# Kernel tuning notes

Hardware: AMD Instinct MI355X
Metric: run time of the kernel (lower is better)

The kernel has to match this reference:

```python
import jax, jax.numpy as jnp
import numpy as np

B, S, E, H, DK = 4, 1024, 1024, 16, 64
FF = 2048
SCALE = int(np.sqrt(DK))  # source uses int(np.sqrt(keySize)) = 8
EPS = 1e-5


def _mha(x_kv, x_q, Wq, Wk, Wv, Wo, mask):
    # Wq/Wk/Wv: [H, E, DK]; Wo: [H*DK, E]
    k = jnp.einsum('bse,hed->hbsd', x_kv, Wk)   # [H,B,S,DK]
    v = jnp.einsum('bse,hed->hbsd', x_kv, Wv)
    q = jnp.einsum('bse,hed->hbsd', x_q, Wq)
    # source does keys.reshape(B, DK, S) -- a RAW reshape, not a transpose
    kR = k.reshape(H, B, DK, S)
    scores = jnp.einsum('hbsd,hbdt->hbst', q, kR)  # [H,B,S,S]
    if mask is not None:
        scores = scores + mask  # mask added BEFORE the scale divide, as in source
    att = jax.nn.softmax(scores / SCALE, axis=-1)
    out = jnp.einsum('hbst,hbtd->hbsd', att, v)    # [H,B,S,DK]
    # source stacks heads then does a RAW reshape [H,B,S,DK] -> [B,S,DK*H]
    out = out.reshape(B, S, DK * H)
    return out @ Wo  # [B,S,E]


def _layernorm2d(x, w, b):
    # LayerNorm over last two dims (S, E) with affine params [S, E]
    m = jnp.mean(x, axis=(-2, -1), keepdims=True)
    v = jnp.var(x, axis=(-2, -1), keepdims=True)
    return (x - m) * jax.lax.rsqrt(v + EPS) * w + b


def setup_inputs() -> dict:
    key = jax.random.key(0)
    ks = jax.random.split(key, 24)
    u = lambda k, shp: jax.random.uniform(k, shp, dtype=jnp.float32)  # weights ~ U(0,1) as in source
    inp = {
        'inputRes': jax.random.normal(ks[0], (B, S, E), dtype=jnp.float32),
        'outputEncoding': jax.random.normal(ks[1], (B, S, E), dtype=jnp.float32),
        'Wq1': u(ks[2], (H, E, DK)), 'Wk1': u(ks[3], (H, E, DK)), 'Wv1': u(ks[4], (H, E, DK)),
        'Wo1': u(ks[5], (H * DK, E)),
        'Wq2': u(ks[6], (H, E, DK)), 'Wk2': u(ks[7], (H, E, DK)), 'Wv2': u(ks[8], (H, E, DK)),
        'Wo2': u(ks[9], (H * DK, E)),
        'ln1_w': jnp.ones((S, E), jnp.float32), 'ln1_b': jnp.zeros((S, E), jnp.float32),
        'ln2_w': jnp.ones((S, E), jnp.float32), 'ln2_b': jnp.zeros((S, E), jnp.float32),
        'ln3_w': jnp.ones((S, E), jnp.float32), 'ln3_b': jnp.zeros((S, E), jnp.float32),
        'W1': jax.random.normal(ks[10], (S, FF), dtype=jnp.float32) * (1.0 / np.sqrt(S)),
        'b1': jnp.zeros((FF,), jnp.float32),
        'W2': jax.random.normal(ks[11], (FF, S), dtype=jnp.float32) * (1.0 / np.sqrt(FF)),
        'b2': jnp.zeros((S,), jnp.float32),
    }
    return inp


def reference(inputRes, outputEncoding, Wq1, Wk1, Wv1, Wo1, Wq2, Wk2, Wv2, Wo2,
              ln1_w, ln1_b, ln2_w, ln2_b, ln3_w, ln3_b, W1, b1, W2, b2):
    # causal mask: row i has 0 for j<=i, -inf for j>i
    idx = jnp.arange(S)
    mask = jnp.where(idx[None, :] <= idx[:, None], 0.0, -jnp.inf).astype(jnp.float32)

    # masked self-attention + residual + LN1
    att = _mha(outputEncoding, outputEncoding, Wq1, Wk1, Wv1, Wo1, mask)
    att_norm = _layernorm2d(att + outputEncoding, ln1_w, ln1_b)

    # cross-attention (K,V from inputRes; Q from att_norm) + residual to outputEncoding + LN2
    att2 = _mha(inputRes, att_norm, Wq2, Wk2, Wv2, Wo2, None)
    att2_norm = _layernorm2d(att2 + outputEncoding, ln2_w, ln2_b)

    # FFN over the sequence dim via RAW reshape (B,S,E)->(B,E,S), as in source
    norm_res = att2_norm.reshape(B, E, S)
    fc = jax.nn.relu(norm_res @ W1 + b1) @ W2 + b2  # [B,E,S]
    fc = fc.reshape(B, S, E)

    return _layernorm2d(fc + att2_norm, ln3_w, ln3_b)
```

## Files before the change

kernel.cpp:

```cpp
#include <hip/hip_runtime.h>
#include <cstdint>
#include <cstddef>


#define DI __device__ __forceinline__
#define MFMA __builtin_amdgcn_mfma_f32_16x16x32_bf16

typedef short s8v __attribute__((ext_vector_type(8)));
typedef float f4v __attribute__((ext_vector_type(4)));
typedef unsigned u4v __attribute__((ext_vector_type(4)));

DI float bf2f(short u){
  union { unsigned int i; float f; } v;
  v.i = ((unsigned int)(unsigned short)u) << 16;
  return v.f;
}
DI short f2bf(float f){
  union { float f; unsigned int i; } v; v.f = f;
  unsigned int x = v.i;
  return (short)((x + 0x7fffu + ((x >> 16) & 1u)) >> 16);
}
DI unsigned pack2(short hi, short lo){
  return ((unsigned)(unsigned short)lo << 16) | (unsigned)(unsigned short)hi;
}
DI unsigned packf(float val){
  short hi = f2bf(val);
  return pack2(hi, f2bf(val - bf2f(hi)));
}
DI void gload16(const void* g, void* l){
  __builtin_amdgcn_global_load_lds(
      (const __attribute__((address_space(1))) unsigned*)g,
      (__attribute__((address_space(3))) unsigned*)l, 16, 0, 0);
}

struct SplitP { const float* src[2]; short* hi[2]; short* lo[2]; };

__launch_bounds__(256)
__global__ void splitall_k(SplitP sp){
  const int t = blockIdx.y;
  int i = (blockIdx.x * 256 + threadIdx.x) << 2;
  float4 v = *(const float4*)(sp.src[t] + i);
  float xs[4] = {v.x, v.y, v.z, v.w};
  short h[4], l[4];
  #pragma unroll
  for (int c = 0; c < 4; c++){
    h[c] = f2bf(xs[c]);
    l[c] = f2bf(xs[c] - bf2f(h[c]));
  }
  *(short4*)(sp.hi[t] + i) = make_short4(h[0], h[1], h[2], h[3]);
  *(short4*)(sp.lo[t] + i) = make_short4(l[0], l[1], l[2], l[3]);
}

struct TransP {
  const float* src[10];
  short* oh[10]; short* ol[10];
  int Kd[10]; int Nd[10]; int qkv[10]; int ntiles[10];
};

__launch_bounds__(256)
__global__ void transall_k(TransP tp){
  const int t = blockIdx.y;
  const int tile = blockIdx.x;
  if (tile >= tp.ntiles[t]) return;
  const int K = tp.Kd[t], N = tp.Nd[t];
  const int ncols = N >> 6;
  const int n0 = (tile % ncols) << 6, k0 = (tile / ncols) << 6;
  __shared__ float Ld[64 * 65];
  const int tid = threadIdx.x;
  const int row = tid >> 2, c16 = (tid & 3) << 4;
  const float* s = tp.src[t];
  size_t base;
  if (tp.qkv[t]) base = ((size_t)(n0 >> 6) << 16) + ((size_t)(k0 + row) << 6) + c16;
  else           base = (size_t)(k0 + row) * N + n0 + c16;
  #pragma unroll
  for (int j4 = 0; j4 < 4; j4++){
    float4 v = *(const float4*)(s + base + (j4 << 2));
    int c = row * 65 + c16 + (j4 << 2);
    Ld[c] = v.x; Ld[c + 1] = v.y; Ld[c + 2] = v.z; Ld[c + 3] = v.w;
  }
  __syncthreads();
  const int n = tid >> 2;
  s8v h0, h1, l0, l1;
  #pragma unroll
  for (int j = 0; j < 8; j++){
    float a = Ld[(c16 + j) * 65 + n];
    float b = Ld[(c16 + 8 + j) * 65 + n];
    short ha = f2bf(a), hb = f2bf(b);
    h0[j] = ha; l0[j] = f2bf(a - bf2f(ha));
    h1[j] = hb; l1[j] = f2bf(b - bf2f(hb));
  }
  size_t ob = (size_t)(n0 + n) * K + k0 + c16;
  *(s8v*)(tp.oh[t] + ob)     = h0;
  *(s8v*)(tp.oh[t] + ob + 8) = h1;
  *(s8v*)(tp.ol[t] + ob)     = l0;
  *(s8v*)(tp.ol[t] + ob + 8) = l1;
}

struct GemmP {
  const short* Ah; const short* Al; int lda;
  const short* Bh; const short* Bl; int ldb;
  int K; int N;
  const float* xres; const float* bias;
  float* outf;
  short* o1h; short* o1l;
  unsigned* p1; unsigned* p2; unsigned* p3;
};

template<int TM, int EPI, int TERMS>
__launch_bounds__(512, 2)
__global__ void gemm_k(GemmP p){
  constexpr int AGR = TM * 4;
  constexpr int NGRAN = (TERMS == 3 ? 2 * AGR : AGR) + 1024;
  constexpr int NG = NGRAN >> 9;
  constexpr int WM = TM >> 6;
  constexpr int NB = 128 / (8 / WM) / 16;
  __shared__ short AhL[3][TM * 32];
  __shared__ short AlL[3][(TERMS == 3) ? TM * 32 : 8];
  __shared__ short BhL[3][128 * 32];
  __shared__ short BlL[3][128 * 32];
  const int tid = threadIdx.x;
  const int L = tid & 63, w = tid >> 6;
  const int lr = L & 15, lg = L >> 4;
  const int mo = (w & (WM - 1)) << 6;
  const int no = (w / WM) * (NB << 4);

  const int gx = gridDim.x, gy = gridDim.y;
  const int f = blockIdx.y * gx + blockIdx.x;
  const int j = f >> 3;
  const int jm = j / gx;
  const int mb = (f & 7) * (gy >> 3) + jm;
  const int nb = j - jm * gx;
  const int m0 = mb * TM, n0 = nb << 7;

  const int lrow4 = L >> 2, lq = L & 3;

  int aoff[4], boff[NB];
  #pragma unroll
  for (int mi = 0; mi < 4; mi++){
    int r = mo + (mi << 4) + lr;
    aoff[mi] = (r << 5) + ((lg ^ ((r >> 1) & 3)) << 3);
  }
  #pragma unroll
  for (int ni = 0; ni < NB; ni++){
    int n = no + (ni << 4) + lr;
    boff[ni] = (n << 5) + ((lg ^ ((n >> 1) & 3)) << 3);
  }

  f4v acc[4][NB];
  #pragma unroll
  for (int i = 0; i < 4; i++)
    #pragma unroll
    for (int jj = 0; jj < NB; jj++)
      #pragma unroll
      for (int r = 0; r < 4; r++) acc[i][jj][r] = 0.0f;

  const int nkt = p.K >> 5;

  auto stage = [&](int tile, int slot){
    const int k0 = tile << 5;
    #pragma unroll
    for (int i = 0; i < NG; i++){
      int base_c = (i << 9) + (w << 6);
      const short* plane; short* lds; int row0; int ld; int pc;
      if (base_c < AGR){
        pc = base_c; plane = p.Ah; lds = &AhL[slot][0]; row0 = m0; ld = p.lda;
      } else if (TERMS == 3 && base_c < 2 * AGR){
        pc = base_c - AGR; plane = p.Al; lds = &AlL[slot][0]; row0 = m0; ld = p.lda;
      } else {
        int pc2 = base_c - (TERMS == 3 ? 2 * AGR : AGR);
        if (pc2 < 512){ pc = pc2; plane = p.Bh; lds = &BhL[slot][0]; }
        else          { pc = pc2 - 512; plane = p.Bl; lds = &BlL[slot][0]; }
        row0 = n0; ld = p.ldb;
      }
      int rl = (pc >> 2) + lrow4;
      int sc = (lq ^ ((rl >> 1) & 3)) << 3;
      gload16(plane + (size_t)(row0 + rl) * ld + k0 + sc, lds + (pc << 3));
    }
  };

  stage(0, 0);
  stage(1, 1);

  for (int kt = 0; kt < nkt; kt++){
    const int cur = kt % 3;
    asm volatile("s_waitcnt vmcnt(%0)\n\ts_barrier" :: "i"(NG) : "memory");

    s8v a_h[4], a_l[4], b_h[NB], b_l[NB];
    #pragma unroll
    for (int mi = 0; mi < 4; mi++){
      a_h[mi] = *(const s8v*)&AhL[cur][aoff[mi]];
      if (TERMS == 3) a_l[mi] = *(const s8v*)&AlL[cur][aoff[mi]];
    }
    #pragma unroll
    for (int ni = 0; ni < NB; ni++){
      b_h[ni] = *(const s8v*)&BhL[cur][boff[ni]];
      b_l[ni] = *(const s8v*)&BlL[cur][boff[ni]];
    }

    int nt = kt + 2 < nkt ? kt + 2 : nkt - 1;
    stage(nt, (kt + 2) % 3);

    #pragma unroll
    for (int ni = 0; ni < NB; ni++){
      #pragma unroll
      for (int mi = 0; mi < 4; mi++){
        acc[mi][ni] = MFMA(a_h[mi], b_h[ni], acc[mi][ni], 0, 0, 0);
        acc[mi][ni] = MFMA(a_h[mi], b_l[ni], acc[mi][ni], 0, 0, 0);
        if (TERMS == 3)
          acc[mi][ni] = MFMA(a_l[mi], b_h[ni], acc[mi][ni], 0, 0, 0);
      }
    }
  }

  #pragma unroll
  for (int mi = 0; mi < 4; mi++){
    #pragma unroll
    for (int ni = 0; ni < NB; ni++){
      #pragma unroll
      for (int r = 0; r < 4; r++){
        float val = acc[mi][ni][r];
        int m = m0 + mo + (mi << 4) + (lg << 2) + r;
        int n = n0 + no + (ni << 4) + lr;
        if (EPI == 2){
          size_t o = (size_t)m * p.N + n;
          p.outf[o] = val + p.xres[o];
        } else if (EPI == 4){
          p.outf[(size_t)m * p.N + n] = val + p.bias[n];
        } else if (EPI == 3){
          float x = val + p.bias[n];
          x = x > 0.0f ? x : 0.0f;
          size_t o = (size_t)m * p.N + n;
          short hi = f2bf(x);
          p.o1h[o] = hi;
          p.o1l[o] = f2bf(x - bf2f(hi));
        } else {
          int seg = (EPI == 0) ? 0 : (n >> 10);
          int n1 = (EPI == 0) ? n : (n & 1023);
          int kind = (EPI == 0) ? 0 : (EPI == 6 ? seg : seg + 1);
          int b = m >> 10, s = m & 1023, hh = n1 >> 6, d = n1 & 63;
          size_t hb16 = (size_t)((hh << 2) | b) << 16;
          size_t dst;
          if (kind == 0)      dst = hb16 + ((size_t)s << 6) + d;
          else if (kind == 1) dst = hb16 + ((size_t)(((s & 15) << 6) | d) << 6) + (s >> 4);
          else                dst = hb16 + ((size_t)d << 10) + s;
          unsigned* dp = (EPI == 0) ? p.p1
                       : (EPI == 6) ? (seg == 0 ? p.p1 : (seg == 1 ? p.p2 : p.p3))
                                    : (seg == 0 ? p.p1 : p.p2);
          dp[dst] = packf(val);
        }
      }
    }
  }
}

template<int CAUSAL>
__launch_bounds__(256, 2)
__global__ void flash_k(const unsigned* __restrict__ qpk,
                        const unsigned* __restrict__ kpk,
                        const unsigned* __restrict__ vpk,
                        short* __restrict__ ohi_g, short* __restrict__ olo_g){
  __shared__ short Kt[2][64*72];
  __shared__ short Vt[2][64*72];
  __shared__ unsigned Ps[2][4][16*68];
  const int tid = threadIdx.x, L = tid & 63, w = tid >> 6;
  const int lr = L & 15, lg = L >> 4;
  const int flat = blockIdx.x + (blockIdx.y << 3);
  const int hb = ((flat & 7) << 3) | ((flat >> 3) & 7);
  const int sp = flat >> 6;
  const int h = hb >> 2, b = hb & 3;
  const size_t hbo = (size_t)hb << 16;
  const float NEG_INF = -__builtin_inff();
  int qt[2]; qt[0] = sp; qt[1] = CAUSAL ? (15 - sp) : (sp + 8);

  s8v qfh[2][2], qfl[2][2];
  #pragma unroll
  for (int st = 0; st < 2; st++){
    const unsigned* qg = qpk + hbo + (size_t)((qt[st] << 6) + (w << 4) + lr) * 64 + (lg << 3);
    #pragma unroll
    for (int ks = 0; ks < 2; ks++){
      u4v p0 = *(const u4v*)(qg + (ks << 5));
      u4v p1 = *(const u4v*)(qg + (ks << 5) + 4);
      #pragma unroll
      for (int jj = 0; jj < 4; jj++){
        qfh[st][ks][jj]     = (short)(p0[jj] & 0xffffu);
        qfl[st][ks][jj]     = (short)(p0[jj] >> 16);
        qfh[st][ks][4 + jj] = (short)(p1[jj] & 0xffffu);
        qfl[st][ks][4 + jj] = (short)(p1[jj] >> 16);
      }
    }
  }

  f4v o[2][4];
  float mprev[2][4], lsum[2][4];
  #pragma unroll
  for (int st = 0; st < 2; st++){
    #pragma unroll
    for (int ni = 0; ni < 4; ni++)
      #pragma unroll
      for (int r = 0; r < 4; r++) o[st][ni][r] = 0.0f;
    #pragma unroll
    for (int r = 0; r < 4; r++){ mprev[st][r] = NEG_INF; lsum[st][r] = 0.0f; }
  }

  const int ntt = CAUSAL ? (qt[1] + 1) : 16;
  for (int ti = 0; ti < ntt; ti++){
    const int t0 = ti << 6;
    const bool actA = !(CAUSAL && ti > qt[0]);
    __syncthreads();
    {
      const int row = tid >> 2, col = (tid & 3) << 4;
      const unsigned* kg = kpk + hbo + (size_t)(t0 + row) * 64 + col;
      const unsigned* vg = vpk + hbo + ((size_t)row << 10) + t0 + col;
      unsigned kb[16], vb[16];
      #pragma unroll
      for (int j4 = 0; j4 < 4; j4++){
        *(u4v*)&kb[j4 << 2] = *(const u4v*)(kg + (j4 << 2));
        *(u4v*)&vb[j4 << 2] = *(const u4v*)(vg + (j4 << 2));
      }
      s8v kh0, kh1, kl0, kl1, vh0, vh1, vl0, vl1;
      #pragma unroll
      for (int jj = 0; jj < 8; jj++){
        kh0[jj] = (short)(kb[jj] & 0xffffu);      kl0[jj] = (short)(kb[jj] >> 16);
        kh1[jj] = (short)(kb[8 + jj] & 0xffffu);  kl1[jj] = (short)(kb[8 + jj] >> 16);
        vh0[jj] = (short)(vb[jj] & 0xffffu);      vl0[jj] = (short)(vb[jj] >> 16);
        vh1[jj] = (short)(vb[8 + jj] & 0xffffu);  vl1[jj] = (short)(vb[8 + jj] >> 16);
      }
      const int lb = row * 72 + col;
      *(s8v*)&Kt[0][lb] = kh0;  *(s8v*)&Kt[0][lb + 8] = kh1;
      *(s8v*)&Kt[1][lb] = kl0;  *(s8v*)&Kt[1][lb + 8] = kl1;
      *(s8v*)&Vt[0][lb] = vh0;  *(s8v*)&Vt[0][lb + 8] = vh1;
      *(s8v*)&Vt[1][lb] = vl0;  *(s8v*)&Vt[1][lb + 8] = vl1;
    }
    __syncthreads();

    f4v sa[2][4];
    #pragma unroll
    for (int st = 0; st < 2; st++)
      #pragma unroll
      for (int ni = 0; ni < 4; ni++)
        #pragma unroll
        for (int r = 0; r < 4; r++) sa[st][ni][r] = 0.0f;
    #pragma unroll
    for (int ks = 0; ks < 2; ks++){
      const int kb = (ks << 5) + (lg << 3);
      #pragma unroll
      for (int ni = 0; ni < 4; ni++){
        const int tl = (ni << 4) + lr;
        s8v kbh = *(const s8v*)&Kt[0][tl * 72 + kb];
        s8v kbl = *(const s8v*)&Kt[1][tl * 72 + kb];
        if (actA){
          sa[0][ni] = MFMA(qfh[0][ks], kbh, sa[0][ni], 0, 0, 0);
          sa[0][ni] = MFMA(qfh[0][ks], kbl, sa[0][ni], 0, 0, 0);
          sa[0][ni] = MFMA(qfl[0][ks], kbh, sa[0][ni], 0, 0, 0);
        }
        sa[1][ni] = MFMA(qfh[1][ks], kbh, sa[1][ni], 0, 0, 0);
        sa[1][ni] = MFMA(qfh[1][ks], kbl, sa[1][ni], 0, 0, 0);
        sa[1][ni] = MFMA(qfl[1][ks], kbh, sa[1][ni], 0, 0, 0);
      }
    }

    #pragma unroll
    for (int st = 0; st < 2; st++){
      if (st == 0 && !actA) continue;
      const int s0w = (qt[st] << 6) + (w << 4);
      const bool diag = CAUSAL && (ti == qt[st]);
      float tm[4] = {NEG_INF, NEG_INF, NEG_INF, NEG_INF};
      #pragma unroll
      for (int ni = 0; ni < 4; ni++)
        #pragma unroll
        for (int r = 0; r < 4; r++){
          float v = sa[st][ni][r] * 0.125f;
          if (diag){
            int tg = t0 + (ni << 4) + lr;
            int sg = s0w + (lg << 2) + r;
            if (tg > sg) v = NEG_INF;
          }
          sa[st][ni][r] = v;
          tm[r] = fmaxf(tm[r], v);
        }
      #pragma unroll
      for (int off = 1; off < 16; off <<= 1)
        #pragma unroll
        for (int r = 0; r < 4; r++) tm[r] = fmaxf(tm[r], __shfl_xor(tm[r], off, 16));
      float alpha[4], psum[4];
      #pragma unroll
      for (int r = 0; r < 4; r++){
        float mn = fmaxf(mprev[st][r], tm[r]);
        alpha[r] = __expf(mprev[st][r] - mn);
        mprev[st][r] = mn;
        psum[r] = 0.0f;
      }
      #pragma unroll
      for (int ni = 0; ni < 4; ni++)
        #pragma unroll
        for (int r = 0; r < 4; r++){
          float pv = __expf(sa[st][ni][r] - mprev[st][r]);
          sa[st][ni][r] = pv;
          psum[r] += pv;
        }
      #pragma unroll
      for (int off = 1; off < 16; off <<= 1)
        #pragma unroll
        for (int r = 0; r < 4; r++) psum[r] += __shfl_xor(psum[r], off, 16);
      #pragma unroll
      for (int r = 0; r < 4; r++) lsum[st][r] = lsum[st][r] * alpha[r] + psum[r];
      #pragma unroll
      for (int ni = 0; ni < 4; ni++)
        #pragma unroll
        for (int r = 0; r < 4; r++) o[st][ni][r] *= alpha[r];
      #pragma unroll
      for (int ni = 0; ni < 4; ni++)
        #pragma unroll
        for (int r = 0; r < 4; r++){
          int prow = (lg << 2) + r, pcol = (ni << 4) + lr;
          Ps[st][w][prow * 68 + pcol] = packf(sa[st][ni][r]);
        }
    }

    #pragma unroll
    for (int ks = 0; ks < 2; ks++){
      const int kb = (ks << 5) + (lg << 3);
      s8v ph[2], pl[2];
      #pragma unroll
      for (int st = 0; st < 2; st++){
        if (st == 0 && !actA) continue;
        u4v p0 = *(const u4v*)&Ps[st][w][lr * 68 + kb];
        u4v p1 = *(const u4v*)&Ps[st][w][lr * 68 + kb + 4];
        #pragma unroll
        for (int jj = 0; jj < 4; jj++){
          ph[st][jj]     = (short)(p0[jj] & 0xffffu);  pl[st][jj]     = (short)(p0[jj] >> 16);
          ph[st][4 + jj] = (short)(p1[jj] & 0xffffu);  pl[st][4 + jj] = (short)(p1[jj] >> 16);
        }
      }
      #pragma unroll
      for (int ni = 0; ni < 4; ni++){
        const int d = (ni << 4) + lr;
        s8v vbh = *(const s8v*)&Vt[0][d * 72 + kb];
        s8v vbl = *(const s8v*)&Vt[1][d * 72 + kb];
        if (actA){
          o[0][ni] = MFMA(ph[0], vbh, o[0][ni], 0, 0, 0);
          o[0][ni] = MFMA(ph[0], vbl, o[0][ni], 0, 0, 0);
          o[0][ni] = MFMA(pl[0], vbh, o[0][ni], 0, 0, 0);
        }
        o[1][ni] = MFMA(ph[1], vbh, o[1][ni], 0, 0, 0);
        o[1][ni] = MFMA(ph[1], vbl, o[1][ni], 0, 0, 0);
        o[1][ni] = MFMA(pl[1], vbh, o[1][ni], 0, 0, 0);
      }
    }
  }

  #pragma unroll
  for (int st = 0; st < 2; st++){
    const int s0w = (qt[st] << 6) + (w << 4);
    #pragma unroll
    for (int ni = 0; ni < 4; ni++){
      #pragma unroll
      for (int r = 0; r < 4; r++){
        float val = o[st][ni][r] / lsum[st][r];
        int s = s0w + (lg << 2) + r;
        int d = (ni << 4) + lr;
        int s2i = ((h & 3) << 8) | (b << 6) | (s >> 4);
        int c   = ((s & 15) << 6) | d;
        size_t dst = ((size_t)(h >> 2) << 20) + ((size_t)s2i << 10) + c;
        short hi = f2bf(val);
        ohi_g[dst] = hi;
        olo_g[dst] = f2bf(val - bf2f(hi));
      }
    }
  }
}

__launch_bounds__(256)
__global__ void ln_partial_k(const float* s1, const float* s2, float2* part){
  const int tid = threadIdx.x, L = tid & 63, w = tid >> 6;
  const int b = blockIdx.y, j = blockIdx.x;
  const size_t base = ((size_t)b << 20) + ((size_t)j << 13) + ((size_t)tid << 2);
  float sum = 0.0f, ss = 0.0f;
  #pragma unroll
  for (int i = 0; i < 8; i++){
    size_t idx = base + ((size_t)i << 10);
    float4 v = *(const float4*)(s1 + idx);
    if (s2){
      float4 u = *(const float4*)(s2 + idx);
      v.x += u.x; v.y += u.y; v.z += u.z; v.w += u.w;
    }
    sum += v.x + v.y + v.z + v.w;
    ss  += v.x*v.x + v.y*v.y + v.z*v.z + v.w*v.w;
  }
  #pragma unroll
  for (int off = 1; off < 64; off <<= 1){
    sum += __shfl_xor(sum, off, 64);
    ss  += __shfl_xor(ss,  off, 64);
  }
  __shared__ float red[4][2];
  if (L == 0){ red[w][0] = sum; red[w][1] = ss; }
  __syncthreads();
  if (tid == 0){
    float s_ = red[0][0] + red[1][0] + red[2][0] + red[3][0];
    float q_ = red[0][1] + red[1][1] + red[2][1] + red[3][1];
    part[b * 128 + j] = make_float2(s_, q_);
  }
}

__launch_bounds__(64)
__global__ void ln_final_k(const float2* part, float2* stats){
  const int b = blockIdx.x, t = threadIdx.x;
  float2 a = part[b * 128 + t], c = part[b * 128 + 64 + t];
  float sum = a.x + c.x, ss = a.y + c.y;
  #pragma unroll
  for (int off = 1; off < 64; off <<= 1){
    sum += __shfl_xor(sum, off, 64);
    ss  += __shfl_xor(ss,  off, 64);
  }
  if (t == 0){
    float mean = sum * (1.0f / 1048576.0f);
    float var  = ss  * (1.0f / 1048576.0f) - mean * mean;
    stats[b] = make_float2(mean, rsqrtf(var + 1e-5f));
  }
}

template<int MODE>
__launch_bounds__(256)
__global__ void ln_apply_k(const float* s1, const float* s2,
                           const float* wgt, const float* bias,
                           const float2* stats,
                           float* dstf, short* dsta, short* dstb){
  const int tid = threadIdx.x;
  const size_t base = ((size_t)blockIdx.x << 11) + ((size_t)tid << 2);
  #pragma unroll
  for (int i = 0; i < 2; i++){
    size_t idx = base + ((size_t)i << 10);
    int b = (int)(idx >> 20);
    float2 st = stats[b];
    float4 x = *(const float4*)(s1 + idx);
    if (s2){
      float4 u = *(const float4*)(s2 + idx);
      x.x += u.x; x.y += u.y; x.z += u.z; x.w += u.w;
    }
    unsigned wi = (unsigned)(idx & 1048575u);
    float4 wv = *(const float4*)(wgt + wi);
    float4 bv = *(const float4*)(bias + wi);
    float xv[4] = {x.x, x.y, x.z, x.w};
    float wvv[4] = {wv.x, wv.y, wv.z, wv.w};
    float bvv[4] = {bv.x, bv.y, bv.z, bv.w};
    float yv[4];
    #pragma unroll
    for (int c = 0; c < 4; c++)
      yv[c] = (xv[c] - st.x) * st.y * wvv[c] + bvv[c];
    if (MODE == 0 || MODE == 1){
      short h[4], l[4];
      #pragma unroll
      for (int c = 0; c < 4; c++){
        h[c] = f2bf(yv[c]);
        l[c] = f2bf(yv[c] - bf2f(h[c]));
      }
      *(short4*)(dsta + idx) = make_short4(h[0], h[1], h[2], h[3]);
      *(short4*)(dstb + idx) = make_short4(l[0], l[1], l[2], l[3]);
      if (MODE == 1)
        *(float4*)(dstf + idx) = make_float4(yv[0], yv[1], yv[2], yv[3]);
    } else {
      *(float4*)(dstf + idx) = make_float4(yv[0], yv[1], yv[2], yv[3]);
    }
  }
}

extern "C" void kernel_launch(void* const* d_in, const int* in_sizes, int n_in,
                              void* d_out, int out_size, void* d_ws, size_t ws_size,
                              hipStream_t stream){
  const float* IRf = (const float*)d_in[0];
  const float* OEf = (const float*)d_in[1];
  const float* Wq1f = (const float*)d_in[2];
  const float* Wk1f = (const float*)d_in[3];
  const float* Wv1f = (const float*)d_in[4];
  const float* Wo1f = (const float*)d_in[5];
  const float* Wq2f = (const float*)d_in[6];
  const float* Wk2f = (const float*)d_in[7];
  const float* Wv2f = (const float*)d_in[8];
  const float* Wo2f = (const float*)d_in[9];
  const float* ln1w = (const float*)d_in[10];
  const float* ln1b = (const float*)d_in[11];
  const float* ln2w = (const float*)d_in[12];
  const float* ln2b = (const float*)d_in[13];
  const float* ln3w = (const float*)d_in[14];
  const float* ln3b = (const float*)d_in[15];
  const float* W1f = (const float*)d_in[16];
  const float* b1f = (const float*)d_in[17];
  const float* W2f = (const float*)d_in[18];
  const float* b2f = (const float*)d_in[19];
  float* dout = (float*)d_out;

  char* ws = (char*)d_ws;
  const size_t MB = (size_t)1 << 20;
  short* OEh = (short*)(ws + 0*MB),  *OEl = (short*)(ws + 8*MB);
  short* IRh = (short*)(ws + 16*MB), *IRl = (short*)(ws + 24*MB);
  short* QKV1t_h = (short*)(ws + 32*MB), *QKV1t_l = (short*)(ws + 38*MB);
  short* Wo1t_h  = (short*)(ws + 44*MB), *Wo1t_l  = (short*)(ws + 46*MB);
  short* Q2t_h   = (short*)(ws + 48*MB), *Q2t_l   = (short*)(ws + 50*MB);
  short* KV2t_h  = (short*)(ws + 52*MB), *KV2t_l  = (short*)(ws + 56*MB);
  short* Wo2t_h  = (short*)(ws + 60*MB), *Wo2t_l  = (short*)(ws + 62*MB);
  short* W1t_h   = (short*)(ws + 64*MB), *W1t_l   = (short*)(ws + 68*MB);
  short* W2t_h   = (short*)(ws + 72*MB), *W2t_l   = (short*)(ws + 76*MB);
  unsigned* q_pk = (unsigned*)(ws + 80*MB);
  unsigned* k_pk = (unsigned*)(ws + 96*MB);
  unsigned* v_pk = (unsigned*)(ws + 112*MB);
  short* outr_h = (short*)(ws + 128*MB), *outr_l = (short*)(ws + 136*MB);
  float* resid = (float*)(ws + 144*MB);
  short* attn_h = (short*)(ws + 160*MB), *attn_l = (short*)(ws + 168*MB);
  float* att2n_f = (float*)(ws + 176*MB);
  short* hid_h = (short*)(ws + 80*MB);
  short* hid_l = (short*)(ws + 96*MB);
  float* fc    = (float*)(ws + 112*MB);
  short* a2n_h = (short*)(ws + 160*MB);
  short* a2n_l = (short*)(ws + 168*MB);
  float2* part  = (float2*)(ws + 192*MB);
  float2* stats = (float2*)(ws + 192*MB + 65536);

  dim3 blk(256), blkg(512);

  SplitP sp;
  sp.src[0] = OEf; sp.hi[0] = OEh; sp.lo[0] = OEl;
  sp.src[1] = IRf; sp.hi[1] = IRh; sp.lo[1] = IRl;
  splitall_k<<<dim3(4096, 2), blk, 0, stream>>>(sp);

  TransP tp;
  const float* tsrc[10] = {Wq1f, Wk1f, Wv1f, Wo1f, Wq2f, Wk2f, Wv2f, Wo2f, W1f, W2f};
  short* toh[10] = {QKV1t_h, QKV1t_h + (1<<20), QKV1t_h + (2<<20), Wo1t_h,
                    Q2t_h, KV2t_h, KV2t_h + (1<<20), Wo2t_h, W1t_h, W2t_h};
  short* tol[10] = {QKV1t_l, QKV1t_l + (1<<20), QKV1t_l + (2<<20), Wo1t_l,
                    Q2t_l, KV2t_l, KV2t_l + (1<<20), Wo2t_l, W1t_l, W2t_l};
  int tK[10]   = {1024,1024,1024,1024,1024,1024,1024,1024,1024,2048};
  int tN[10]   = {1024,1024,1024,1024,1024,1024,1024,1024,2048,1024};
  int tq[10]   = {1,1,1,0,1,1,1,0,0,0};
  int tt[10]   = {256,256,256,256,256,256,256,256,512,512};
  for (int i = 0; i < 10; i++){
    tp.src[i] = tsrc[i]; tp.oh[i] = toh[i]; tp.ol[i] = tol[i];
    tp.Kd[i] = tK[i]; tp.Nd[i] = tN[i]; tp.qkv[i] = tq[i]; tp.ntiles[i] = tt[i];
  }
  transall_k<<<dim3(512, 10), blk, 0, stream>>>(tp);

  GemmP p{};

  p = {OEh, OEl, 1024, QKV1t_h, QKV1t_l, 1024, 1024, 3072, nullptr, nullptr,
       nullptr, nullptr, nullptr, q_pk, k_pk, v_pk};
  gemm_k<256,6,3><<<dim3(24, 16), blkg, 0, stream>>>(p);
  flash_k<1><<<dim3(8, 64), blk, 0, stream>>>(q_pk, k_pk, v_pk, outr_h, outr_l);
  p = {outr_h, outr_l, 1024, Wo1t_h, Wo1t_l, 1024, 1024, 1024, OEf, nullptr,
       resid, nullptr, nullptr, nullptr, nullptr, nullptr};
  gemm_k<128,2,3><<<dim3(8, 32), blkg, 0, stream>>>(p);
  ln_partial_k<<<dim3(128, 4), blk, 0, stream>>>(resid, nullptr, part);
  ln_final_k<<<dim3(4), dim3(64), 0, stream>>>(part, stats);
  ln_apply_k<0><<<dim3(2048), blk, 0, stream>>>(resid, nullptr, ln1w, ln1b, stats, nullptr, attn_h, attn_l);

  p = {attn_h, attn_l, 1024, Q2t_h, Q2t_l, 1024, 1024, 1024, nullptr, nullptr,
       nullptr, nullptr, nullptr, q_pk, nullptr, nullptr};
  gemm_k<128,0,3><<<dim3(8, 32), blkg, 0, stream>>>(p);
  p = {IRh, IRl, 1024, KV2t_h, KV2t_l, 1024, 1024, 2048, nullptr, nullptr,
       nullptr, nullptr, nullptr, k_pk, v_pk, nullptr};
  gemm_k<256,7,3><<<dim3(16, 16), blkg, 0, stream>>>(p);
  flash_k<0><<<dim3(8, 64), blk, 0, stream>>>(q_pk, k_pk, v_pk, outr_h, outr_l);
  p = {outr_h, outr_l, 1024, Wo2t_h, Wo2t_l, 1024, 1024, 1024, OEf, nullptr,
       resid, nullptr, nullptr, nullptr, nullptr, nullptr};
  gemm_k<128,2,3><<<dim3(8, 32), blkg, 0, stream>>>(p);
  ln_partial_k<<<dim3(128, 4), blk, 0, stream>>>(resid, nullptr, part);
  ln_final_k<<<dim3(4), dim3(64), 0, stream>>>(part, stats);
  ln_apply_k<1><<<dim3(2048), blk, 0, stream>>>(resid, nullptr, ln2w, ln2b, stats, att2n_f, a2n_h, a2n_l);

  p = {a2n_h, a2n_l, 1024, W1t_h, W1t_l, 1024, 1024, 2048, nullptr, b1f,
       nullptr, hid_h, hid_l, nullptr, nullptr, nullptr};
  gemm_k<256,3,2><<<dim3(16, 16), blkg, 0, stream>>>(p);
  p = {hid_h, hid_l, 2048, W2t_h, W2t_l, 2048, 2048, 1024, nullptr, b2f,
       fc, nullptr, nullptr, nullptr, nullptr, nullptr};
  gemm_k<128,4,2><<<dim3(8, 32), blkg, 0, stream>>>(p);
  ln_partial_k<<<dim3(128, 4), blk, 0, stream>>>(fc, att2n_f, part);
  ln_final_k<<<dim3(4), dim3(64), 0, stream>>>(part, stats);
  ln_apply_k<2><<<dim3(2048), blk, 0, stream>>>(fc, att2n_f, ln3w, ln3b, stats, dout, nullptr, nullptr);
}
```

Baseline: 690.7 us.

## Add 128x128 256-thread GEMM variant with double buffering for wide GEMMs

Adds a new GEMM kernel using 128x128 tiles, 256 threads (4 waves, each computing 64x64) and two-stage LDS buffering with a full vmcnt(0) wait. The QKV1, KV2 and FFN1 projections switch from the 256-row, 512-thread triple-buffered kernel to it, doubling the grid. The goal is more blocks per CU and better wave balance across CUs with less LDS per block. In exchange, the pipeline is shallower and the kernel waits for all loads every iteration, which may expose memory latency. The epilogue is moved into a shared helper.

```diff
diff --git a/kernel.cpp b/kernel.cpp
--- a/kernel.cpp
+++ b/kernel.cpp
@@ -106,112 +106,9 @@
   unsigned* p1; unsigned* p2; unsigned* p3;
 };
 
-template<int TM, int EPI, int TERMS>
-__launch_bounds__(512, 2)
-__global__ void gemm_k(GemmP p){
-  constexpr int AGR = TM * 4;
-  constexpr int NGRAN = (TERMS == 3 ? 2 * AGR : AGR) + 1024;
-  constexpr int NG = NGRAN >> 9;
-  constexpr int WM = TM >> 6;
-  constexpr int NB = 128 / (8 / WM) / 16;
-  __shared__ short AhL[3][TM * 32];
-  __shared__ short AlL[3][(TERMS == 3) ? TM * 32 : 8];
-  __shared__ short BhL[3][128 * 32];
-  __shared__ short BlL[3][128 * 32];
-  const int tid = threadIdx.x;
-  const int L = tid & 63, w = tid >> 6;
-  const int lr = L & 15, lg = L >> 4;
-  const int mo = (w & (WM - 1)) << 6;
-  const int no = (w / WM) * (NB << 4);
-
-  const int gx = gridDim.x, gy = gridDim.y;
-  const int f = blockIdx.y * gx + blockIdx.x;
-  const int j = f >> 3;
-  const int jm = j / gx;
-  const int mb = (f & 7) * (gy >> 3) + jm;
-  const int nb = j - jm * gx;
-  const int m0 = mb * TM, n0 = nb << 7;
-
-  const int lrow4 = L >> 2, lq = L & 3;
-
-  int aoff[4], boff[NB];
-  #pragma unroll
-  for (int mi = 0; mi < 4; mi++){
-    int r = mo + (mi << 4) + lr;
-    aoff[mi] = (r << 5) + ((lg ^ ((r >> 1) & 3)) << 3);
-  }
-  #pragma unroll
-  for (int ni = 0; ni < NB; ni++){
-    int n = no + (ni << 4) + lr;
-    boff[ni] = (n << 5) + ((lg ^ ((n >> 1) & 3)) << 3);
-  }
-
-  f4v acc[4][NB];
-  #pragma unroll
-  for (int i = 0; i < 4; i++)
-    #pragma unroll
-    for (int jj = 0; jj < NB; jj++)
-      #pragma unroll
-      for (int r = 0; r < 4; r++) acc[i][jj][r] = 0.0f;
-
-  const int nkt = p.K >> 5;
-
-  auto stage = [&](int tile, int slot){
-    const int k0 = tile << 5;
-    #pragma unroll
-    for (int i = 0; i < NG; i++){
-      int base_c = (i << 9) + (w << 6);
-      const short* plane; short* lds; int row0; int ld; int pc;
-      if (base_c < AGR){
-        pc = base_c; plane = p.Ah; lds = &AhL[slot][0]; row0 = m0; ld = p.lda;
-      } else if (TERMS == 3 && base_c < 2 * AGR){
-        pc = base_c - AGR; plane = p.Al; lds = &AlL[slot][0]; row0 = m0; ld = p.lda;
-      } else {
-        int pc2 = base_c - (TERMS == 3 ? 2 * AGR : AGR);
-        if (pc2 < 512){ pc = pc2; plane = p.Bh; lds = &BhL[slot][0]; }
-        else          { pc = pc2 - 512; plane = p.Bl; lds = &BlL[slot][0]; }
-        row0 = n0; ld = p.ldb;
-      }
-      int rl = (pc >> 2) + lrow4;
-      int sc = (lq ^ ((rl >> 1) & 3)) << 3;
-      gload16(plane + (size_t)(row0 + rl) * ld + k0 + sc, lds + (pc << 3));
-    }
-  };
-
-  stage(0, 0);
-  stage(1, 1);
-
-  for (int kt = 0; kt < nkt; kt++){
-    const int cur = kt % 3;
-    asm volatile("s_waitcnt vmcnt(%0)\n\ts_barrier" :: "i"(NG) : "memory");
-
-    s8v a_h[4], a_l[4], b_h[NB], b_l[NB];
-    #pragma unroll
-    for (int mi = 0; mi < 4; mi++){
-      a_h[mi] = *(const s8v*)&AhL[cur][aoff[mi]];
-      if (TERMS == 3) a_l[mi] = *(const s8v*)&AlL[cur][aoff[mi]];
-    }
-    #pragma unroll
-    for (int ni = 0; ni < NB; ni++){
-      b_h[ni] = *(const s8v*)&BhL[cur][boff[ni]];
-      b_l[ni] = *(const s8v*)&BlL[cur][boff[ni]];
-    }
-
-    int nt = kt + 2 < nkt ? kt + 2 : nkt - 1;
-    stage(nt, (kt + 2) % 3);
-
-    #pragma unroll
-    for (int ni = 0; ni < NB; ni++){
-      #pragma unroll
-      for (int mi = 0; mi < 4; mi++){
-        acc[mi][ni] = MFMA(a_h[mi], b_h[ni], acc[mi][ni], 0, 0, 0);
-        acc[mi][ni] = MFMA(a_h[mi], b_l[ni], acc[mi][ni], 0, 0, 0);
-        if (TERMS == 3)
-          acc[mi][ni] = MFMA(a_l[mi], b_h[ni], acc[mi][ni], 0, 0, 0);
-      }
-    }
-  }
-
+template<int EPI, int NB>
+DI void gemm_epilogue(const GemmP& p, f4v (&acc)[4][NB],
+                      int m0, int n0, int mo, int no, int lr, int lg){
   #pragma unroll
   for (int mi = 0; mi < 4; mi++){
     #pragma unroll
@@ -253,6 +150,220 @@
   }
 }
 
+template<int TM, int EPI, int TERMS>
+__launch_bounds__(512, 2)
+__global__ void gemm_k(GemmP p){
+  constexpr int AGR = TM * 4;
+  constexpr int NGRAN = (TERMS == 3 ? 2 * AGR : AGR) + 1024;
+  constexpr int NG = NGRAN >> 9;
+  constexpr int WM = TM >> 6;
+  constexpr int NB = 128 / (8 / WM) / 16;
+  __shared__ short AhL[3][TM * 32];
+  __shared__ short AlL[3][(TERMS == 3) ? TM * 32 : 8];
+  __shared__ short BhL[3][128 * 32];
+  __shared__ short BlL[3][128 * 32];
+  const int tid = threadIdx.x;
+  const int L = tid & 63, w = tid >> 6;
+  const int lr = L & 15, lg = L >> 4;
+  const int mo = (w & (WM - 1)) << 6;
+  const int no = (w / WM) * (NB << 4);
+
+  const int gx = gridDim.x, gy = gridDim.y;
+  const int f = blockIdx.y * gx + blockIdx.x;
+  const int j = f >> 3;
+  const int jm = j / gx;
+  const int mb = (f & 7) * (gy >> 3) + jm;
+  const int nb = j - jm * gx;
+  const int m0 = mb * TM, n0 = nb << 7;
+
+  const int lrow4 = L >> 2, lq = L & 3;
+
+  int aoff[4], boff[NB];
+  #pragma unroll
+  for (int mi = 0; mi < 4; mi++){
+    int r = mo + (mi << 4) + lr;
+    aoff[mi] = (r << 5) + ((lg ^ ((r >> 1) & 3)) << 3);
+  }
+  #pragma unroll
+  for (int ni = 0; ni < NB; ni++){
+    int n = no + (ni << 4) + lr;
+    boff[ni] = (n << 5) + ((lg ^ ((n >> 1) & 3)) << 3);
+  }
+
+  f4v acc[4][NB];
+  #pragma unroll
+  for (int i = 0; i < 4; i++)
+    #pragma unroll
+    for (int jj = 0; jj < NB; jj++)
+      #pragma unroll
+      for (int r = 0; r < 4; r++) acc[i][jj][r] = 0.0f;
+
+  const int nkt = p.K >> 5;
+
+  auto stage = [&](int tile, int slot){
+    const int k0 = tile << 5;
+    #pragma unroll
+    for (int i = 0; i < NG; i++){
+      int base_c = (i << 9) + (w << 6);
+      const short* plane; short* lds; int row0; int ld; int pc;
+      if (base_c < AGR){
+        pc = base_c; plane = p.Ah; lds = &AhL[slot][0]; row0 = m0; ld = p.lda;
+      } else if (TERMS == 3 && base_c < 2 * AGR){
+        pc = base_c - AGR; plane = p.Al; lds = &AlL[slot][0]; row0 = m0; ld = p.lda;
+      } else {
+        int pc2 = base_c - (TERMS == 3 ? 2 * AGR : AGR);
+        if (pc2 < 512){ pc = pc2; plane = p.Bh; lds = &BhL[slot][0]; }
+        else          { pc = pc2 - 512; plane = p.Bl; lds = &BlL[slot][0]; }
+        row0 = n0; ld = p.ldb;
+      }
+      int rl = (pc >> 2) + lrow4;
+      int sc = (lq ^ ((rl >> 1) & 3)) << 3;
+      gload16(plane + (size_t)(row0 + rl) * ld + k0 + sc, lds + (pc << 3));
+    }
+  };
+
+  stage(0, 0);
+  stage(1, 1);
+
+  for (int kt = 0; kt < nkt; kt++){
+    const int cur = kt % 3;
+    asm volatile("s_waitcnt vmcnt(%0)\n\ts_barrier" :: "i"(NG) : "memory");
+
+    s8v a_h[4], a_l[4], b_h[NB], b_l[NB];
+    #pragma unroll
+    for (int mi = 0; mi < 4; mi++){
+      a_h[mi] = *(const s8v*)&AhL[cur][aoff[mi]];
+      if (TERMS == 3) a_l[mi] = *(const s8v*)&AlL[cur][aoff[mi]];
+    }
+    #pragma unroll
+    for (int ni = 0; ni < NB; ni++){
+      b_h[ni] = *(const s8v*)&BhL[cur][boff[ni]];
+      b_l[ni] = *(const s8v*)&BlL[cur][boff[ni]];
+    }
+
+    int nt = kt + 2 < nkt ? kt + 2 : nkt - 1;
+    stage(nt, (kt + 2) % 3);
+
+    #pragma unroll
+    for (int ni = 0; ni < NB; ni++){
+      #pragma unroll
+      for (int mi = 0; mi < 4; mi++){
+        acc[mi][ni] = MFMA(a_h[mi], b_h[ni], acc[mi][ni], 0, 0, 0);
+        acc[mi][ni] = MFMA(a_h[mi], b_l[ni], acc[mi][ni], 0, 0, 0);
+        if (TERMS == 3)
+          acc[mi][ni] = MFMA(a_l[mi], b_h[ni], acc[mi][ni], 0, 0, 0);
+      }
+    }
+  }
+
+  gemm_epilogue<EPI, NB>(p, acc, m0, n0, mo, no, lr, lg);
+}
+
+template<int EPI, int TERMS>
+__launch_bounds__(256, 2)
+__global__ void gemm2_k(GemmP p){
+  constexpr int AGR = 512;
+  constexpr int NGRAN = (TERMS == 3 ? 2 * AGR : AGR) + 1024;
+  constexpr int NG = NGRAN >> 8;
+  constexpr int NB = 4;
+  __shared__ short AhL[2][128 * 32];
+  __shared__ short AlL[2][(TERMS == 3) ? 128 * 32 : 8];
+  __shared__ short BhL[2][128 * 32];
+  __shared__ short BlL[2][128 * 32];
+  const int tid = threadIdx.x;
+  const int L = tid & 63, w = tid >> 6;
+  const int lr = L & 15, lg = L >> 4;
+  const int mo = (w & 1) << 6;
+  const int no = (w >> 1) << 6;
+
+  const int gx = gridDim.x, gy = gridDim.y;
+  const int f = blockIdx.y * gx + blockIdx.x;
+  const int j = f >> 3;
+  const int jm = j / gx;
+  const int mb = (f & 7) * (gy >> 3) + jm;
+  const int nb = j - jm * gx;
+  const int m0 = mb << 7, n0 = nb << 7;
+
+  const int lrow4 = L >> 2, lq = L & 3;
+
+  int aoff[4], boff[NB];
+  #pragma unroll
+  for (int mi = 0; mi < 4; mi++){
+    int r = mo + (mi << 4) + lr;
+    aoff[mi] = (r << 5) + ((lg ^ ((r >> 1) & 3)) << 3);
+  }
+  #pragma unroll
+  for (int ni = 0; ni < NB; ni++){
+    int n = no + (ni << 4) + lr;
+    boff[ni] = (n << 5) + ((lg ^ ((n >> 1) & 3)) << 3);
+  }
+
+  f4v acc[4][NB];
+  #pragma unroll
+  for (int i = 0; i < 4; i++)
+    #pragma unroll
+    for (int jj = 0; jj < NB; jj++)
+      #pragma unroll
+      for (int r = 0; r < 4; r++) acc[i][jj][r] = 0.0f;
+
+  const int nkt = p.K >> 5;
+
+  auto stage = [&](int tile, int slot){
+    const int k0 = tile << 5;
+    #pragma unroll
+    for (int i = 0; i < NG; i++){
+      int base_c = (i << 8) + (w << 6);
+      const short* plane; short* lds; int row0; int ld; int pc;
+      if (base_c < AGR){
+        pc = base_c; plane = p.Ah; lds = &AhL[slot][0]; row0 = m0; ld = p.lda;
+      } else if (TERMS == 3 && base_c < 2 * AGR){
+        pc = base_c - AGR; plane = p.Al; lds = &AlL[slot][0]; row0 = m0; ld = p.lda;
+      } else {
+        int pc2 = base_c - (TERMS == 3 ? 2 * AGR : AGR);
+        if (pc2 < 512){ pc = pc2; plane = p.Bh; lds = &BhL[slot][0]; }
+        else          { pc = pc2 - 512; plane = p.Bl; lds = &BlL[slot][0]; }
+        row0 = n0; ld = p.ldb;
+      }
+      int rl = (pc >> 2) + lrow4;
+      int sc = (lq ^ ((rl >> 1) & 3)) << 3;
+      gload16(plane + (size_t)(row0 + rl) * ld + k0 + sc, lds + (pc << 3));
+    }
+  };
+
+  stage(0, 0);
+
+  for (int kt = 0; kt < nkt; kt++){
+    const int cur = kt & 1;
+    asm volatile("s_waitcnt vmcnt(0)\n\ts_barrier" ::: "memory");
+    if (kt + 1 < nkt) stage(kt + 1, cur ^ 1);
+
+    s8v a_h[4], a_l[4], b_h[NB], b_l[NB];
+    #pragma unroll
+    for (int mi = 0; mi < 4; mi++){
+      a_h[mi] = *(const s8v*)&AhL[cur][aoff[mi]];
+      if (TERMS == 3) a_l[mi] = *(const s8v*)&AlL[cur][aoff[mi]];
+    }
+    #pragma unroll
+    for (int ni = 0; ni < NB; ni++){
+      b_h[ni] = *(const s8v*)&BhL[cur][boff[ni]];
+      b_l[ni] = *(const s8v*)&BlL[cur][boff[ni]];
+    }
+
+    #pragma unroll
+    for (int ni = 0; ni < NB; ni++){
+      #pragma unroll
+      for (int mi = 0; mi < 4; mi++){
+        acc[mi][ni] = MFMA(a_h[mi], b_h[ni], acc[mi][ni], 0, 0, 0);
+        acc[mi][ni] = MFMA(a_h[mi], b_l[ni], acc[mi][ni], 0, 0, 0);
+        if (TERMS == 3)
+          acc[mi][ni] = MFMA(a_l[mi], b_h[ni], acc[mi][ni], 0, 0, 0);
+      }
+    }
+  }
+
+  gemm_epilogue<EPI, NB>(p, acc, m0, n0, mo, no, lr, lg);
+}
+
 template<int CAUSAL>
 __launch_bounds__(256, 2)
 __global__ void flash_k(const unsigned* __restrict__ qpk,
@@ -642,7 +753,7 @@
 
   p = {OEh, OEl, 1024, QKV1t_h, QKV1t_l, 1024, 1024, 3072, nullptr, nullptr,
        nullptr, nullptr, nullptr, q_pk, k_pk, v_pk};
-  gemm_k<256,6,3><<<dim3(24, 16), blkg, 0, stream>>>(p);
+  gemm2_k<6,3><<<dim3(24, 32), blk, 0, stream>>>(p);
   flash_k<1><<<dim3(8, 64), blk, 0, stream>>>(q_pk, k_pk, v_pk, outr_h, outr_l);
   p = {outr_h, outr_l, 1024, Wo1t_h, Wo1t_l, 1024, 1024, 1024, OEf, nullptr,
        resid, nullptr, nullptr, nullptr, nullptr, nullptr};
@@ -656,7 +767,7 @@
   gemm_k<128,0,3><<<dim3(8, 32), blkg, 0, stream>>>(p);
   p = {IRh, IRl, 1024, KV2t_h, KV2t_l, 1024, 1024, 2048, nullptr, nullptr,
        nullptr, nullptr, nullptr, k_pk, v_pk, nullptr};
-  gemm_k<256,7,3><<<dim3(16, 16), blkg, 0, stream>>>(p);
+  gemm2_k<7,3><<<dim3(16, 32), blk, 0, stream>>>(p);
   flash_k<0><<<dim3(8, 64), blk, 0, stream>>>(q_pk, k_pk, v_pk, outr_h, outr_l);
   p = {outr_h, outr_l, 1024, Wo2t_h, Wo2t_l, 1024, 1024, 1024, OEf, nullptr,
        resid, nullptr, nullptr, nullptr, nullptr, nullptr};
@@ -667,7 +778,7 @@
 
   p = {a2n_h, a2n_l, 1024, W1t_h, W1t_l, 1024, 1024, 2048, nullptr, b1f,
        nullptr, hid_h, hid_l, nullptr, nullptr, nullptr};
-  gemm_k<256,3,2><<<dim3(16, 16), blkg, 0, stream>>>(p);
+  gemm2_k<3,2><<<dim3(16, 32), blk, 0, stream>>>(p);
   p = {hid_h, hid_l, 2048, W2t_h, W2t_l, 2048, 2048, 1024, nullptr, b2f,
        fc, nullptr, nullptr, nullptr, nullptr, nullptr};
   gemm_k<128,4,2><<<dim3(8, 32), blkg, 0, stream>>>(p);
```

Result: slower. 764.6 us (+10.7%).

## Fuse layernorm statistics into GEMM epilogues via atomic per-batch accumulators

Applied to the files above, without the earlier changes.

Each output GEMM epilogue now accumulates sum and sum-of-squares of its output tile, reduces them across the block, and atomically adds them into a per-batch float2 accumulator zeroed by a memset. This removes the ln_partial and ln_final kernels, and the extra full-tensor read they needed, for all three layernorms. The FFN second GEMM also folds in the residual add, so the final apply no longer reads a second tensor. In exchange, the variance comes from a single-pass E[x^2]-mean^2 over atomics whose order is not fixed, which is nondeterministic and more prone to cancellation.

```diff
diff --git a/kernel.cpp b/kernel.cpp
--- a/kernel.cpp
+++ b/kernel.cpp
@@ -104,6 +104,7 @@
   float* outf;
   short* o1h; short* o1l;
   unsigned* p1; unsigned* p2; unsigned* p3;
+  float2* sacc;
 };
 
 template<int TM, int EPI, int TERMS>
@@ -212,6 +213,7 @@
     }
   }
 
+  float ls = 0.0f, lss = 0.0f;
   #pragma unroll
   for (int mi = 0; mi < 4; mi++){
     #pragma unroll
@@ -223,7 +225,14 @@
         int n = n0 + no + (ni << 4) + lr;
         if (EPI == 2){
           size_t o = (size_t)m * p.N + n;
-          p.outf[o] = val + p.xres[o];
+          float x = val + p.xres[o];
+          p.outf[o] = x;
+          ls += x; lss += x * x;
+        } else if (EPI == 5){
+          size_t o = (size_t)m * p.N + n;
+          float x = val + p.bias[n] + p.xres[o];
+          p.outf[o] = x;
+          ls += x; lss += x * x;
         } else if (EPI == 4){
           p.outf[(size_t)m * p.N + n] = val + p.bias[n];
         } else if (EPI == 3){
@@ -251,6 +260,24 @@
       }
     }
   }
+
+  if (EPI == 2 || EPI == 5){
+    #pragma unroll
+    for (int off = 1; off < 64; off <<= 1){
+      ls  += __shfl_xor(ls,  off, 64);
+      lss += __shfl_xor(lss, off, 64);
+    }
+    __shared__ float sred[8][2];
+    if (L == 0){ sred[w][0] = ls; sred[w][1] = lss; }
+    __syncthreads();
+    if (tid == 0){
+      float s_ = 0.0f, q_ = 0.0f;
+      #pragma unroll
+      for (int i = 0; i < 8; i++){ s_ += sred[i][0]; q_ += sred[i][1]; }
+      atomicAdd(&p.sacc[m0 >> 10].x, s_);
+      atomicAdd(&p.sacc[m0 >> 10].y, q_);
+    }
+  }
 }
 
 template<int CAUSAL>
@@ -470,60 +497,11 @@
   }
 }
 
-__launch_bounds__(256)
-__global__ void ln_partial_k(const float* s1, const float* s2, float2* part){
-  const int tid = threadIdx.x, L = tid & 63, w = tid >> 6;
-  const int b = blockIdx.y, j = blockIdx.x;
-  const size_t base = ((size_t)b << 20) + ((size_t)j << 13) + ((size_t)tid << 2);
-  float sum = 0.0f, ss = 0.0f;
-  #pragma unroll
-  for (int i = 0; i < 8; i++){
-    size_t idx = base + ((size_t)i << 10);
-    float4 v = *(const float4*)(s1 + idx);
-    if (s2){
-      float4 u = *(const float4*)(s2 + idx);
-      v.x += u.x; v.y += u.y; v.z += u.z; v.w += u.w;
-    }
-    sum += v.x + v.y + v.z + v.w;
-    ss  += v.x*v.x + v.y*v.y + v.z*v.z + v.w*v.w;
-  }
-  #pragma unroll
-  for (int off = 1; off < 64; off <<= 1){
-    sum += __shfl_xor(sum, off, 64);
-    ss  += __shfl_xor(ss,  off, 64);
-  }
-  __shared__ float red[4][2];
-  if (L == 0){ red[w][0] = sum; red[w][1] = ss; }
-  __syncthreads();
-  if (tid == 0){
-    float s_ = red[0][0] + red[1][0] + red[2][0] + red[3][0];
-    float q_ = red[0][1] + red[1][1] + red[2][1] + red[3][1];
-    part[b * 128 + j] = make_float2(s_, q_);
-  }
-}
-
-__launch_bounds__(64)
-__global__ void ln_final_k(const float2* part, float2* stats){
-  const int b = blockIdx.x, t = threadIdx.x;
-  float2 a = part[b * 128 + t], c = part[b * 128 + 64 + t];
-  float sum = a.x + c.x, ss = a.y + c.y;
-  #pragma unroll
-  for (int off = 1; off < 64; off <<= 1){
-    sum += __shfl_xor(sum, off, 64);
-    ss  += __shfl_xor(ss,  off, 64);
-  }
-  if (t == 0){
-    float mean = sum * (1.0f / 1048576.0f);
-    float var  = ss  * (1.0f / 1048576.0f) - mean * mean;
-    stats[b] = make_float2(mean, rsqrtf(var + 1e-5f));
-  }
-}
-
 template<int MODE>
 __launch_bounds__(256)
 __global__ void ln_apply_k(const float* s1, const float* s2,
                            const float* wgt, const float* bias,
-                           const float2* stats,
+                           const float2* sacc,
                            float* dstf, short* dsta, short* dstb){
   const int tid = threadIdx.x;
   const size_t base = ((size_t)blockIdx.x << 11) + ((size_t)tid << 2);
@@ -531,7 +509,9 @@
   for (int i = 0; i < 2; i++){
     size_t idx = base + ((size_t)i << 10);
     int b = (int)(idx >> 20);
-    float2 st = stats[b];
+    float2 sp = sacc[b];
+    float mean = sp.x * (1.0f / 1048576.0f);
+    float rstd = rsqrtf(sp.y * (1.0f / 1048576.0f) - mean * mean + 1e-5f);
     float4 x = *(const float4*)(s1 + idx);
     if (s2){
       float4 u = *(const float4*)(s2 + idx);
@@ -546,7 +526,7 @@
     float yv[4];
     #pragma unroll
     for (int c = 0; c < 4; c++)
-      yv[c] = (xv[c] - st.x) * st.y * wvv[c] + bvv[c];
+      yv[c] = (xv[c] - mean) * rstd * wvv[c] + bvv[c];
     if (MODE == 0 || MODE == 1){
       short h[4], l[4];
       #pragma unroll
@@ -613,9 +593,10 @@
   short* a2n_h = (short*)(ws + 160*MB);
   short* a2n_l = (short*)(ws + 168*MB);
   float2* part  = (float2*)(ws + 192*MB);
-  float2* stats = (float2*)(ws + 192*MB + 65536);
 
   dim3 blk(256), blkg(512);
+
+  hipMemsetAsync(part, 0, 12 * sizeof(float2), stream);
 
   SplitP sp;
   sp.src[0] = OEf; sp.hi[0] = OEh; sp.lo[0] = OEl;
@@ -641,37 +622,31 @@
   GemmP p{};
 
   p = {OEh, OEl, 1024, QKV1t_h, QKV1t_l, 1024, 1024, 3072, nullptr, nullptr,
-       nullptr, nullptr, nullptr, q_pk, k_pk, v_pk};
+       nullptr, nullptr, nullptr, q_pk, k_pk, v_pk, nullptr};
   gemm_k<256,6,3><<<dim3(24, 16), blkg, 0, stream>>>(p);
   flash_k<1><<<dim3(8, 64), blk, 0, stream>>>(q_pk, k_pk, v_pk, outr_h, outr_l);
   p = {outr_h, outr_l, 1024, Wo1t_h, Wo1t_l, 1024, 1024, 1024, OEf, nullptr,
-       resid, nullptr, nullptr, nullptr, nullptr, nullptr};
+       resid, nullptr, nullptr, nullptr, nullptr, nullptr, part};
   gemm_k<128,2,3><<<dim3(8, 32), blkg, 0, stream>>>(p);
-  ln_partial_k<<<dim3(128, 4), blk, 0, stream>>>(resid, nullptr, part);
-  ln_final_k<<<dim3(4), dim3(64), 0, stream>>>(part, stats);
-  ln_apply_k<0><<<dim3(2048), blk, 0, stream>>>(resid, nullptr, ln1w, ln1b, stats, nullptr, attn_h, attn_l);
+  ln_apply_k<0><<<dim3(2048), blk, 0, stream>>>(resid, nullptr, ln1w, ln1b, part, nullptr, attn_h, attn_l);
 
   p = {attn_h, attn_l, 1024, Q2t_h, Q2t_l, 1024, 1024, 1024, nullptr, nullptr,
-       nullptr, nullptr, nullptr, q_pk, nullptr, nullptr};
+       nullptr, nullptr, nullptr, q_pk, nullptr, nullptr, nullptr};
   gemm_k<128,0,3><<<dim3(8, 32), blkg, 0, stream>>>(p);
   p = {IRh, IRl, 1024, KV2t_h, KV2t_l, 1024, 1024, 2048, nullptr, nullptr,
-       nullptr, nullptr, nullptr, k_pk, v_pk, nullptr};
+       nullptr, nullptr, nullptr, k_pk, v_pk, nullptr, nullptr};
   gemm_k<256,7,3><<<dim3(16, 16), blkg, 0, stream>>>(p);
   flash_k<0><<<dim3(8, 64), blk, 0, stream>>>(q_pk, k_pk, v_pk, outr_h, outr_l);
   p = {outr_h, outr_l, 1024, Wo2t_h, Wo2t_l, 1024, 1024, 1024, OEf, nullptr,
-       resid, nullptr, nullptr, nullptr, nullptr, nullptr};
+       resid, nullptr, nullptr, nullptr, nullptr, nullptr, part + 4};
   gemm_k<128,2,3><<<dim3(8, 32), blkg, 0, stream>>>(p);
-  ln_partial_k<<<dim3(128, 4), blk, 0, stream>>>(resid, nullptr, part);
-  ln_final_k<<<dim3(4), dim3(64), 0, stream>>>(part, stats);
-  ln_apply_k<1><<<dim3(2048), blk, 0, stream>>>(resid, nullptr, ln2w, ln2b, stats, att2n_f, a2n_h, a2n_l);
+  ln_apply_k<1><<<dim3(2048), blk, 0, stream>>>(resid, nullptr, ln2w, ln2b, part + 4, att2n_f, a2n_h, a2n_l);
 
   p = {a2n_h, a2n_l, 1024, W1t_h, W1t_l, 1024, 1024, 2048, nullptr, b1f,
-       nullptr, hid_h, hid_l, nullptr, nullptr, nullptr};
+       nullptr, hid_h, hid_l, nullptr, nullptr, nullptr, nullptr};
   gemm_k<256,3,2><<<dim3(16, 16), blkg, 0, stream>>>(p);
-  p = {hid_h, hid_l, 2048, W2t_h, W2t_l, 2048, 2048, 1024, nullptr, b2f,
-       fc, nullptr, nullptr, nullptr, nullptr, nullptr};
-  gemm_k<128,4,2><<<dim3(8, 32), blkg, 0, stream>>>(p);
-  ln_partial_k<<<dim3(128, 4), blk, 0, stream>>>(fc, att2n_f, part);
-  ln_final_k<<<dim3(4), dim3(64), 0, stream>>>(part, stats);
-  ln_apply_k<2><<<dim3(2048), blk, 0, stream>>>(fc, att2n_f, ln3w, ln3b, stats, dout, nullptr, nullptr);
-}
+  p = {hid_h, hid_l, 2048, W2t_h, W2t_l, 2048, 2048, 1024, att2n_f, b2f,
+       fc, nullptr, nullptr, nullptr, nullptr, nullptr, part + 8};
+  gemm_k<128,5,2><<<dim3(8, 32), blkg, 0, stream>>>(p);
+  ln_apply_k<2><<<dim3(2048), blk, 0, stream>>>(fc, nullptr, ln3w, ln3b, part + 8, dout, nullptr, nullptr);
+}
```

Result: slower. 736.6 us (median of 2 runs) (+6.6%).
